# Performance work log

Hardware: AMD Instinct MI355X
Metric: run time of the kernel (lower is better)

## Reference

```python
import jax, jax.numpy as jnp
import numpy as np

K, NC, NA = 9, 13, 5
NB, NH, NW = 128, 26, 26
NT, L = 50, 2 * K + 3
NOOBJ, OBJ, SIL = 1.0, 5.0, 0.6
COORD_S, CLASS_S = 1.0, 1.0
PRETRAIN_EPOCHS = 15
TH, SHARP = 80.0, 2.0                      # corner-conf distance threshold (px), sharpness
SCALE = np.array([640.0, 480.0], np.float32)  # im_width, im_height used by corner_confidences
CONF0 = float(np.exp(SHARP) - 1.0)
ANCHORS = np.array([1.482, 2.2412, 2.0501, 3.1265, 2.3946, 4.6891,
                    3.1018, 3.991, 3.4879, 5.8851], np.float32).reshape(NA, 2)


def setup_inputs():
    k1, k2 = jax.random.split(jax.random.key(0))
    output = jax.random.normal(k1, (NB, NA * (2 * K + 1 + NC), NH, NW), dtype=jnp.float32)
    target = jax.random.uniform(k2, (NB, NT * L), dtype=jnp.float32)
    return {"output": output, "target": target, "epoch": 20}


def _corner_conf(pred, gt):
    # pred, gt: [..., K, 2] normalized corners -> mean per-corner confidence [...]
    d = jnp.sqrt((((pred - gt) * jnp.asarray(SCALE)) ** 2).sum(-1))  # pixel distance [..., K]
    c = (jnp.exp(SHARP * (1.0 - d / TH)) - 1.0) / CONF0
    return jnp.where(d < TH, c, 0.0).mean(-1)


def _region_loss(output, target, epoch):
    nAnch, nPix = NA * NH * NW, NH * NW
    tgt = jax.lax.stop_gradient(target).reshape(NB, NT, L)
    out = output.reshape(NB, NA, 2 * K + 1 + NC, NH, NW)
    # keypoint 0 gets sigmoid, the rest are raw offsets
    xs = jnp.concatenate([jax.nn.sigmoid(out[:, :, 0:1]), out[:, :, 2:2 * K:2]], axis=2)  # [B,A,K,H,W]
    ys = jnp.concatenate([jax.nn.sigmoid(out[:, :, 1:2]), out[:, :, 3:2 * K:2]], axis=2)
    conf = jax.nn.sigmoid(out[:, :, 2 * K])                             # [B,A,H,W]
    cls_logits = jnp.transpose(out[:, :, 2 * K + 1:], (0, 1, 3, 4, 2))  # [B,A,H,W,NC]

    gxg = jnp.arange(NW, dtype=jnp.float32)
    gyg = jnp.arange(NH, dtype=jnp.float32)
    px = (jax.lax.stop_gradient(xs) + gxg) / NW            # detached, as torch uses .data
    py = (jax.lax.stop_gradient(ys) + gyg[:, None]) / NH
    # pred corners per anchor cell, flat anchor index = a*H*W + j*W + i -> [B, A*H*W, K, 2]
    pc = jnp.transpose(jnp.stack([px, py], -1), (0, 1, 3, 4, 2, 5)).reshape(NB, nAnch, K, 2)

    gt_xy = tgt[:, :, 1:1 + 2 * K].reshape(NB, NT, K, 2)
    # torch loop breaks at first target with x1 == 0 -> cumulative validity
    valid = jnp.cumprod((tgt[:, :, 1] != 0).astype(jnp.int32), axis=1) > 0  # [B,T]

    # pass 1: max corner confidence over valid GT, per anchor cell
    def max_conf_step(cur, inp):
        gt_t, v_t = inp                                    # [B,K,2], [B]
        c = _corner_conf(pc, gt_t[:, None]).reshape(NB, NA, NH, NW)
        return jnp.where(v_t[:, None, None, None], jnp.maximum(cur, c), cur), None

    cur_confs, _ = jax.lax.scan(max_conf_step, jnp.zeros((NB, NA, NH, NW), jnp.float32),
                                (jnp.swapaxes(gt_xy, 0, 1), valid.T))
    conf_mask0 = jnp.where(cur_confs > SIL, 0.0, NOOBJ)

    # per-target quantities (vectorized over b,t)
    gx = gt_xy[..., 0] * NW                                # [B,T,K]
    gy = gt_xy[..., 1] * NH
    gi0 = jnp.clip(jnp.floor(gx[:, :, 0]).astype(jnp.int32), 0, NW - 1)  # [B,T]
    gj0 = jnp.clip(jnp.floor(gy[:, :, 0]).astype(jnp.int32), 0, NH - 1)
    # pred_box is fetched with best_n == -1 (as in the source); emulate torch negative flat index via mod
    flat_idx = jnp.mod(jnp.arange(NB)[:, None] * nAnch - nPix + gj0 * NW + gi0, NB * nAnch)
    pred_box = pc.reshape(NB * nAnch, K, 2)[flat_idx]      # [B,T,K,2]
    conf_t = _corner_conf(pred_box, gt_xy)                 # [B,T]
    gw = tgt[:, :, L - 2] * NW
    gh = tgt[:, :, L - 1] * NH
    aw, ah = ANCHORS[:, 0], ANCHORS[:, 1]
    mw = jnp.minimum(aw, gw[..., None])                    # centered-box IoU (bbox_iou, cxcywh)
    mh = jnp.minimum(ah, gh[..., None])
    inter = mw * mh
    iou = inter / (aw * ah + (gw * gh)[..., None] - inter)
    best_n = jnp.argmax(iou, axis=-1).astype(jnp.int32)    # [B,T] (first max, like strict '>')
    txv = gx - gi0[..., None].astype(jnp.float32)          # [B,T,K]
    tyv = gy - gj0[..., None].astype(jnp.float32)
    tclsv = tgt[:, :, 0]

    # pass 2: sequential scatter matching torch overwrite order over t
    barange = jnp.arange(NB)
    z = jnp.zeros((NB, NA, NH, NW), jnp.float32)
    zk = jnp.zeros((NB, NA, NH, NW, K), jnp.float32)

    def scatter_step(carry, inp):
        cm, clm, cfm, tx, ty, tcf, tcl = carry
        v, bn, gj, gi, cft, txt, tyt, tct = inp
        idx = (barange, bn, gj, gi)
        vk = v[:, None]
        cm = cm.at[idx].set(jnp.where(v, 1.0, cm[idx]))
        clm = clm.at[idx].set(jnp.where(v, 1.0, clm[idx]))
        cfm = cfm.at[idx].set(jnp.where(v, OBJ, cfm[idx]))
        tx = tx.at[idx].set(jnp.where(vk, txt, tx[idx]))
        ty = ty.at[idx].set(jnp.where(vk, tyt, ty[idx]))
        tcf = tcf.at[idx].set(jnp.where(v, cft, tcf[idx]))
        tcl = tcl.at[idx].set(jnp.where(v, tct, tcl[idx]))
        return (cm, clm, cfm, tx, ty, tcf, tcl), None

    inps = (valid.T, best_n.T, gj0.T, gi0.T, conf_t.T,
            jnp.swapaxes(txv, 0, 1), jnp.swapaxes(tyv, 0, 1), tclsv.T)
    (coord_mask, cls_mask, conf_mask, tx, ty, tconf, tcls), _ = jax.lax.scan(
        scatter_step, (z, z, conf_mask0, zk, zk, z, z), inps)

    # losses
    xsT = jnp.transpose(xs, (0, 1, 3, 4, 2))               # [B,A,H,W,K]
    ysT = jnp.transpose(ys, (0, 1, 3, 4, 2))
    cmk = coord_mask[..., None]
    loss_x = 0.5 * COORD_S * jnp.sum(((xsT - tx) * cmk) ** 2)
    loss_y = 0.5 * COORD_S * jnp.sum(((ysT - ty) * cmk) ** 2)
    sq = jnp.sqrt(conf_mask)
    loss_conf = 0.5 * jnp.sum(((conf - tconf) * sq) ** 2)
    labels = jnp.clip(tcls.astype(jnp.int32), 0, NC - 1)
    ce = -jnp.take_along_axis(jax.nn.log_softmax(cls_logits, axis=-1),
                              labels[..., None], axis=-1)[..., 0]
    loss_cls = CLASS_S * jnp.sum(ce * cls_mask)
    loss = loss_x + loss_y + loss_cls
    if epoch > PRETRAIN_EPOCHS:
        loss = loss + loss_conf
    return loss


def reference(output, target, epoch):
    return _region_loss(output, target, epoch)
```

## Files before the change

### kernel.cpp

```cpp
#include <hip/hip_runtime.h>
#include <math.h>

#define KK     9
#define NCLS   13
#define NANC   5
#define NBB    128
#define NHH    26
#define NWW    26
#define NTT    50
#define LL     21
#define CHC    32
#define NPIX   676
#define NANCHT 3380
#define NCELLT 432640
#define GTS    20
#define GTH    24
#define MWPB   106
#define HALFSPLIT 1728
#define NBLK   27

#define LOG2E_F   1.4426950408889634f
#define K1C       2.8853900817779268f
#define K2C       0.036067376022224085f
#define SXW       24.615384615384617f
#define SYH       18.461538461538463f
#define THRESH_S  43.500902934225507f
#define CULL_H    330.0f
#define CONF_T_SCALE 0.017390849194407297f
#define OBJ_W     5.0f
#define EPOCH_PRETRAIN 15
#define BIGV      6.0e18f

typedef _Float16 h2 __attribute__((ext_vector_type(2)));
typedef _Float16 h4 __attribute__((ext_vector_type(4)));
typedef _Float16 h8 __attribute__((ext_vector_type(8)));

static __device__ __forceinline__ float fast_exp2(float x){ return __builtin_amdgcn_exp2f(x); }
static __device__ __forceinline__ float fast_sqrt(float x){ return __builtin_amdgcn_sqrtf(x); }
static __device__ __forceinline__ float sigmoidf_(float x){
  return 1.0f/(1.0f + fast_exp2(-LOG2E_F*x));
}

__constant__ float c_anch[10] = {1.482f,2.2412f,2.0501f,3.1265f,2.3946f,4.6891f,
                                 3.1018f,3.991f,3.4879f,5.8851f};


__global__ __launch_bounds__(64) void prep_kernel(const float* __restrict__ tgt,
                                                  float* __restrict__ gts_neg,
                                                  _Float16* __restrict__ gth,
                                                  int* __restrict__ nvalid){
  int b = blockIdx.x;
  int t = threadIdx.x;
  const float* trow = tgt + (size_t)b*NTT*LL;
  float v1 = (t < NTT) ? trow[t*LL + 1] : 0.0f;
  unsigned long long mk = __ballot(t < NTT && v1 != 0.0f);
  int firstInvalid = __ffsll(~mk) - 1;
  if (t == 0) nvalid[b] = firstInvalid;
  for (int idx = t; idx < NTT*GTS; idx += 64){
    int tt = idx / GTS;
    int c  = idx - tt*GTS;
    float v;
    if (c == 9 || c == 19)      v = BIGV;
    else if (c < 9)             v = -(trow[tt*LL + 1 + 2*c] * 640.0f);
    else                        v = -(trow[tt*LL + 2 + 2*(c-10)] * 480.0f);
    gts_neg[(size_t)b*NTT*GTS + idx] = v;
  }
  for (int idx = t; idx < NTT*GTH; idx += 64){
    int tt = idx / GTH;
    int c  = idx - tt*GTH;
    float v = 0.0f;
    if (c < 8)        v = -(trow[tt*LL + 1 + 2*c] * 640.0f);
    else if (c < 16)  v = -(trow[tt*LL + 2 + 2*(c-8)] * 480.0f);
    else if (c == 16) v = -(trow[tt*LL + 1 + 16] * 640.0f);
    else if (c == 17) v = -(trow[tt*LL + 2 + 16] * 480.0f);
    gth[(size_t)b*NTT*GTH + idx] = (_Float16)v;
  }
}

__global__ __launch_bounds__(64) void region_confmask_kernel(
    const float* __restrict__ outp, const _Float16* __restrict__ gth,
    const float* __restrict__ gts_neg, const int* __restrict__ nvalid,
    unsigned int* __restrict__ maskw, double* __restrict__ partials){
  int b = blockIdx.y;
  int tid = threadIdx.x;
  int wavebase0 = blockIdx.x * 64;
  int c0 = wavebase0 + tid;
  int c1 = c0 + HALFSPLIT;
  bool ok1 = (c1 < NANCHT);

  __shared__ int sgt_i[NTT*GTH/2] __attribute__((aligned(16)));
  const int* gsrc = (const int*)(gth + (size_t)b*NTT*GTH);
  for (int idx = tid; idx < NTT*GTH/2; idx += 64) sgt_i[idx] = gsrc[idx];
  __syncthreads();
  const _Float16* sgt = (const _Float16*)sgt_i;

  float Pxf0[KK], Pyf0[KK], Pxf1[KK], Pyf1[KK];
  h8 Px8_0, Py8_0, Px8_1, Py8_1;
  h2 Pt_0, Pt_1;
  float cf0 = 0.0f, cf1 = 0.0f;
#pragma unroll
  for (int k = 0; k < KK; ++k){ Pxf1[k] = 0.0f; Pyf1[k] = 0.0f; }

  {
    int a = c0 / NPIX, rem = c0 - a*NPIX;
    int j = rem / NWW, i = rem - j*NWW;
    const float* base = outp + (((size_t)b*NANC + a)*CHC)*NPIX + rem;
#pragma unroll
    for (int k = 0; k < KK; ++k){
      float rx = base[(2*k)*NPIX], ry = base[(2*k+1)*NPIX];
      if (k == 0){ rx = sigmoidf_(rx); ry = sigmoidf_(ry); }
      Pxf0[k] = (rx + (float)i)*SXW; Pyf0[k] = (ry + (float)j)*SYH;
    }
    cf0 = sigmoidf_(base[(2*KK)*NPIX]);
  }
  if (ok1){
    int a = c1 / NPIX, rem = c1 - a*NPIX;
    int j = rem / NWW, i = rem - j*NWW;
    const float* base = outp + (((size_t)b*NANC + a)*CHC)*NPIX + rem;
#pragma unroll
    for (int k = 0; k < KK; ++k){
      float rx = base[(2*k)*NPIX], ry = base[(2*k+1)*NPIX];
      if (k == 0){ rx = sigmoidf_(rx); ry = sigmoidf_(ry); }
      Pxf1[k] = (rx + (float)i)*SXW; Pyf1[k] = (ry + (float)j)*SYH;
    }
    cf1 = sigmoidf_(base[(2*KK)*NPIX]);
  }
#pragma unroll
  for (int k = 0; k < 8; ++k){
    Px8_0[k] = (_Float16)Pxf0[k]; Py8_0[k] = (_Float16)Pyf0[k];
    Px8_1[k] = (_Float16)Pxf1[k]; Py8_1[k] = (_Float16)Pyf1[k];
  }
  Pt_0 = (h2){(_Float16)Pxf0[8], (_Float16)Pyf0[8]};
  Pt_1 = (h2){(_Float16)Pxf1[8], (_Float16)Pyf1[8]};

  const _Float16 TH16 = (_Float16)CULL_H;
  int nv = nvalid[b];
  unsigned long long q0 = 0ull, q1 = 0ull;
#pragma unroll 2
  for (int t = 0; t < nv; ++t){
    h8 GX = *(const h8*)(sgt + t*GTH);
    h8 GY = *(const h8*)(sgt + t*GTH + 8);
    h2 GT = *(const h2*)(sgt + t*GTH + 16);
    unsigned long long bit = 1ull << t;
    {
      h8 dx = Px8_0 + GX, dy = Py8_0 + GY;
      h8 r  = __builtin_elementwise_fma(dy, dy, dx*dx);
      h4 r4 = __builtin_elementwise_min(__builtin_shufflevector(r, r, 0,1,2,3),
                                        __builtin_shufflevector(r, r, 4,5,6,7));
      h2 r2 = __builtin_elementwise_min(__builtin_shufflevector(r4, r4, 0,1),
                                        __builtin_shufflevector(r4, r4, 2,3));
      h2 dt = Pt_0 + GT; h2 rt = dt*dt;
      _Float16 m = __builtin_elementwise_min(
          __builtin_elementwise_min(r2[0], r2[1]), (_Float16)(rt[0] + rt[1]));
      if (m < TH16) q0 |= bit;
    }
    {
      h8 dx = Px8_1 + GX, dy = Py8_1 + GY;
      h8 r  = __builtin_elementwise_fma(dy, dy, dx*dx);
      h4 r4 = __builtin_elementwise_min(__builtin_shufflevector(r, r, 0,1,2,3),
                                        __builtin_shufflevector(r, r, 4,5,6,7));
      h2 r2 = __builtin_elementwise_min(__builtin_shufflevector(r4, r4, 0,1),
                                        __builtin_shufflevector(r4, r4, 2,3));
      h2 dt = Pt_1 + GT; h2 rt = dt*dt;
      _Float16 m = __builtin_elementwise_min(
          __builtin_elementwise_min(r2[0], r2[1]), (_Float16)(rt[0] + rt[1]));
      if (m < TH16) q1 |= bit;
    }
  }
  if (!ok1) q1 = 0ull;

  int m0_0 = 1, m0_1 = 1;
  if (__any((q0 | q1) != 0ull)){
    const float* gbase = gts_neg + (size_t)b*NTT*GTS;
    bool e0 = false, e1 = false;
    while (q0){
      int t = __ffsll((long long)q0) - 1; q0 &= q0 - 1;
      const float* gg = gbase + t*GTS;
      float s = 0.0f;
#pragma unroll
      for (int k = 0; k < KK; ++k){
        float dx = Pxf0[k] + gg[k], dy = Pyf0[k] + gg[10+k];
        float d  = fast_sqrt(fmaf(dy, dy, dx*dx));
        float e  = fast_exp2(fmaf(d, -K2C, K1C));
        s += fmaxf(e, 1.0f);
      }
      e0 |= (s > THRESH_S);
    }
    while (q1){
      int t = __ffsll((long long)q1) - 1; q1 &= q1 - 1;
      const float* gg = gbase + t*GTS;
      float s = 0.0f;
#pragma unroll
      for (int k = 0; k < KK; ++k){
        float dx = Pxf1[k] + gg[k], dy = Pyf1[k] + gg[10+k];
        float d  = fast_sqrt(fmaf(dy, dy, dx*dx));
        float e  = fast_exp2(fmaf(d, -K2C, K1C));
        s += fmaxf(e, 1.0f);
      }
      e1 |= (s > THRESH_S);
    }
    if (e0) m0_0 = 0;
    if (e1) m0_1 = 0;
  }

  float contrib = (m0_0 ? 0.5f*cf0*cf0 : 0.0f) + ((ok1 && m0_1) ? 0.5f*cf1*cf1 : 0.0f);

  int lane = tid;
  unsigned long long mb0 = __ballot(m0_0 != 0);
  if ((lane & 31) == 0){
    unsigned int w = (lane == 0) ? (unsigned int)mb0 : (unsigned int)(mb0 >> 32);
    maskw[(size_t)b*MWPB + (wavebase0 >> 5) + (lane >> 5)] = w;
  }
  unsigned long long mb1 = __ballot(m0_1 != 0);
  int wavebase1 = wavebase0 + HALFSPLIT;
  if ((lane & 31) == 0 && wavebase1 < NANCHT){
    unsigned int w = (lane == 0) ? (unsigned int)mb1 : (unsigned int)(mb1 >> 32);
    maskw[(size_t)b*MWPB + (wavebase1 >> 5) + (lane >> 5)] = w;
  }

#pragma unroll
  for (int o = 32; o > 0; o >>= 1) contrib += __shfl_xor(contrib, o, 64);
  if (tid == 0) partials[b*NBLK + blockIdx.x] = (double)contrib;
}

__global__ __launch_bounds__(64) void scatter_loss_kernel(
    const float* __restrict__ outp, const float* __restrict__ tgt,
    const int* __restrict__ nvalid, const unsigned int* __restrict__ maskw,
    double* __restrict__ bc_part){
  int b = blockIdx.x;
  int t = threadIdx.x;
  __shared__ int keys[NTT];
  int nv = nvalid[b];
  bool valid = (t < nv);

  int key = -1, gi0 = 0, gj0 = 0, bn = 0;
  float txv[KK], tyv[KK];
  float conf_t = 0.0f, tcls = 0.0f;

  if (t < NTT){
    const float* trow = tgt + ((size_t)b*NTT + t)*LL;
    tcls = trow[0];
    float gx0 = trow[1]*(float)NWW;
    float gy0 = trow[2]*(float)NHH;
    gi0 = min(max((int)floorf(gx0), 0), NWW-1);
    gj0 = min(max((int)floorf(gy0), 0), NHH-1);
#pragma unroll
    for (int k = 0; k < KK; ++k){
      txv[k] = trow[1+2*k]*(float)NWW - (float)gi0;
      tyv[k] = trow[2+2*k]*(float)NHH - (float)gj0;
    }
    float gw = trow[LL-2]*(float)NWW, gh = trow[LL-1]*(float)NHH;
    float best = -1.0f;
    for (int a = 0; a < NANC; ++a){
      float aw = c_anch[2*a], ah = c_anch[2*a+1];
      float inter = fminf(aw, gw) * fminf(ah, gh);
      float iou = inter / (aw*ah + gw*gh - inter);
      if (iou > best){ best = iou; bn = a; }
    }
    key = bn*NPIX + gj0*NWW + gi0;
    keys[t] = key;

    long f = (long)b*NANCHT - NPIX + gj0*NWW + gi0;
    if (f < 0) f += NCELLT;
    int bb  = (int)(f / NANCHT);
    int rr  = (int)(f - (long)bb*NANCHT);
    int aa  = rr / NPIX;
    int rr2 = rr - aa*NPIX;
    int jj  = rr2 / NWW;
    int ii  = rr2 - jj*NWW;
    const float* pbase = outp + (((size_t)bb*NANC + aa)*CHC)*NPIX + rr2;
    float s = 0.0f;
#pragma unroll
    for (int k = 0; k < KK; ++k){
      float rx = pbase[(2*k)*NPIX], ry = pbase[(2*k+1)*NPIX];
      if (k == 0){ rx = sigmoidf_(rx); ry = sigmoidf_(ry); }
      float Pxx = (rx + (float)ii)*SXW, Pyy = (ry + (float)jj)*SYH;
      float dx = Pxx - trow[1+2*k]*640.0f;
      float dy = Pyy - trow[2+2*k]*480.0f;
      float d  = fast_sqrt(fmaf(dy, dy, dx*dx));
      float e  = fast_exp2(fmaf(d, -K2C, K1C));
      s += fmaxf(e, 1.0f);
    }
    conf_t = (s - 9.0f) * CONF_T_SCALE;
  }
  __syncthreads();

  bool winner = valid;
  if (valid){
    for (int u = t+1; u < nv; ++u) if (keys[u] == key){ winner = false; break; }
  }

  double lx = 0.0, ly = 0.0, lcls = 0.0, lcf = 0.0;
  if (winner){
    const float* cbase = outp + (((size_t)b*NANC + bn)*CHC)*NPIX + gj0*NWW + gi0;
    float sx = 0.0f, sy = 0.0f;
#pragma unroll
    for (int k = 0; k < KK; ++k){
      float rx = cbase[(2*k)*NPIX], ry = cbase[(2*k+1)*NPIX];
      if (k == 0){ rx = sigmoidf_(rx); ry = sigmoidf_(ry); }
      float dx = rx - txv[k], dy = ry - tyv[k];
      sx = fmaf(dx, dx, sx); sy = fmaf(dy, dy, sy);
    }
    lx = 0.5*(double)sx; ly = 0.5*(double)sy;

    float lg[NCLS], mx = -1e30f;
#pragma unroll
    for (int c = 0; c < NCLS; ++c){ lg[c] = cbase[(2*KK+1+c)*NPIX]; mx = fmaxf(mx, lg[c]); }
    float se = 0.0f;
#pragma unroll
    for (int c = 0; c < NCLS; ++c) se += fast_exp2((lg[c]-mx)*LOG2E_F);
    int label = min(max((int)tcls, 0), NCLS-1);
    lcls = (double)(mx + logf(se) - lg[label]);

    float cf = sigmoidf_(cbase[(2*KK)*NPIX]);
    int idx = bn*NPIX + gj0*NWW + gi0;
    int m0 = (maskw[(size_t)b*MWPB + (idx >> 5)] >> (idx & 31)) & 1;
    float dcf = cf - conf_t;
    lcf = 0.5*OBJ_W*(double)(dcf*dcf) - (m0 ? 0.5*(double)(cf*cf) : 0.0);
  }

#pragma unroll
  for (int o = 32; o > 0; o >>= 1){
    lx  += __shfl_xor(lx,  o, 64);
    ly  += __shfl_xor(ly,  o, 64);
    lcls+= __shfl_xor(lcls,o, 64);
    lcf += __shfl_xor(lcf, o, 64);
  }
  if (threadIdx.x == 0){
    double* bp = bc_part + (size_t)b*4;
    bp[0] = lx; bp[1] = ly; bp[2] = lcls; bp[3] = lcf;
  }
}

__global__ __launch_bounds__(256) void finalize_kernel(
    const double* __restrict__ bc_part, const double* __restrict__ partials,
    const int* __restrict__ epoch_p, float* __restrict__ outv){
  int tid = threadIdx.x;
  double vx=0, vy=0, vc=0, vf=0, vb=0;
  for (int i = tid; i < NBB; i += 256){
    vx += bc_part[4*i]; vy += bc_part[4*i+1];
    vc += bc_part[4*i+2]; vf += bc_part[4*i+3];
  }
  for (int i = tid; i < NBLK*NBB; i += 256) vb += partials[i];
#pragma unroll
  for (int o = 32; o > 0; o >>= 1){
    vx += __shfl_xor(vx, o, 64); vy += __shfl_xor(vy, o, 64);
    vc += __shfl_xor(vc, o, 64); vf += __shfl_xor(vf, o, 64);
    vb += __shfl_xor(vb, o, 64);
  }
  __shared__ double sm[5][4];
  int wid = tid >> 6, lane = tid & 63;
  if (lane == 0){ sm[0][wid]=vx; sm[1][wid]=vy; sm[2][wid]=vc; sm[3][wid]=vf; sm[4][wid]=vb; }
  __syncthreads();
  if (tid == 0){
    double fx=0, fy=0, fc=0, ff=0, fb=0;
    for (int w = 0; w < 4; ++w){ fx+=sm[0][w]; fy+=sm[1][w]; fc+=sm[2][w]; ff+=sm[3][w]; fb+=sm[4][w]; }
    double loss = fx + fy + fc;
    if (*epoch_p > EPOCH_PRETRAIN) loss += ff + fb;
    outv[0] = (float)loss;
  }
}

extern "C" void kernel_launch(void* const* d_in, const int* in_sizes, int n_in,
                              void* d_out, int out_size, void* d_ws, size_t ws_size,
                              hipStream_t stream){
  (void)in_sizes; (void)n_in; (void)out_size; (void)ws_size;
  const float* outp = (const float*)d_in[0];
  const float* tgt  = (const float*)d_in[1];
  const int*   ep   = (const int*)d_in[2];
  float* outv = (float*)d_out;
  char* ws = (char*)d_ws;

  double* bc_part   = (double*)(ws);
  double* partials  = (double*)(ws + 4096);
  float*  gts_neg   = (float*) (ws + 31744);
  int*    nvalid    = (int*)   (ws + 543744);
  unsigned int* maskw = (unsigned int*)(ws + 544256);
  _Float16* gth     = (_Float16*)(ws + 598528);

  prep_kernel<<<dim3(NBB), dim3(64), 0, stream>>>(tgt, gts_neg, gth, nvalid);
  region_confmask_kernel<<<dim3(NBLK, NBB), dim3(64), 0, stream>>>(outp, gth, gts_neg, nvalid, maskw, partials);
  scatter_loss_kernel<<<dim3(NBB), dim3(64), 0, stream>>>(outp, tgt, nvalid, maskw, bc_part);
  finalize_kernel<<<dim3(1), dim3(256), 0, stream>>>(bc_part, partials, ep, outv);
}
```

Before: 149.4 us.

## Widen confmask blocks, drop fp32 prediction registers, recompute on exact path

Measured after the change: 149.9 us. About the same (+0.3%).

```diff
diff --git a/kernel.cpp b/kernel.cpp
--- a/kernel.cpp
+++ b/kernel.cpp
@@ -16,8 +16,8 @@
 #define GTS    20
 #define GTH    24
 #define MWPB   106
-#define HALFSPLIT 1728
-#define NBLK   27
+#define HALFSPLIT 1792
+#define NBLK   7
 
 #define LOG2E_F   1.4426950408889634f
 #define K1C       2.8853900817779268f
@@ -25,21 +25,22 @@
 #define SXW       24.615384615384617f
 #define SYH       18.461538461538463f
 #define THRESH_S  43.500902934225507f
-#define CULL_H    330.0f
+#define CULL_H    400.0f
 #define CONF_T_SCALE 0.017390849194407297f
 #define OBJ_W     5.0f
 #define EPOCH_PRETRAIN 15
 #define BIGV      6.0e18f
 
 typedef _Float16 h2 __attribute__((ext_vector_type(2)));
-typedef _Float16 h4 __attribute__((ext_vector_type(4)));
-typedef _Float16 h8 __attribute__((ext_vector_type(8)));
+typedef int      i4 __attribute__((ext_vector_type(4)));
 
 static __device__ __forceinline__ float fast_exp2(float x){ return __builtin_amdgcn_exp2f(x); }
 static __device__ __forceinline__ float fast_sqrt(float x){ return __builtin_amdgcn_sqrtf(x); }
 static __device__ __forceinline__ float sigmoidf_(float x){
   return 1.0f/(1.0f + fast_exp2(-LOG2E_F*x));
 }
+static __device__ __forceinline__ h2 bch2(int v){ return __builtin_bit_cast(h2, v); }
+static __device__ __forceinline__ _Float16 hmin(_Float16 a, _Float16 b){ return a < b ? a : b; }
 
 __constant__ float c_anch[10] = {1.482f,2.2412f,2.0501f,3.1265f,2.3946f,4.6891f,
                                  3.1018f,3.991f,3.4879f,5.8851f};
@@ -77,94 +78,97 @@
   }
 }
 
-__global__ __launch_bounds__(64) void region_confmask_kernel(
+__global__ __launch_bounds__(256) void region_confmask_kernel(
     const float* __restrict__ outp, const _Float16* __restrict__ gth,
     const float* __restrict__ gts_neg, const int* __restrict__ nvalid,
     unsigned int* __restrict__ maskw, double* __restrict__ partials){
   int b = blockIdx.y;
   int tid = threadIdx.x;
-  int wavebase0 = blockIdx.x * 64;
-  int c0 = wavebase0 + tid;
+  int c0 = blockIdx.x * 256 + tid;
   int c1 = c0 + HALFSPLIT;
   bool ok1 = (c1 < NANCHT);
 
   __shared__ int sgt_i[NTT*GTH/2] __attribute__((aligned(16)));
   const int* gsrc = (const int*)(gth + (size_t)b*NTT*GTH);
-  for (int idx = tid; idx < NTT*GTH/2; idx += 64) sgt_i[idx] = gsrc[idx];
-  __syncthreads();
+  for (int idx = tid; idx < NTT*GTH/2; idx += 256) sgt_i[idx] = gsrc[idx];
   const _Float16* sgt = (const _Float16*)sgt_i;
 
-  float Pxf0[KK], Pyf0[KK], Pxf1[KK], Pyf1[KK];
-  h8 Px8_0, Py8_0, Px8_1, Py8_1;
-  h2 Pt_0, Pt_1;
-  float cf0 = 0.0f, cf1 = 0.0f;
-#pragma unroll
-  for (int k = 0; k < KK; ++k){ Pxf1[k] = 0.0f; Pyf1[k] = 0.0f; }
-
+  h2 Pxp0[4], Pyp0[4], Pt0, Pxp1[4], Pyp1[4], Pt1;
+  float cf0, cf1 = 0.0f;
   {
     int a = c0 / NPIX, rem = c0 - a*NPIX;
     int j = rem / NWW, i = rem - j*NWW;
     const float* base = outp + (((size_t)b*NANC + a)*CHC)*NPIX + rem;
+    float px8 = 0.0f, py8 = 0.0f;
 #pragma unroll
     for (int k = 0; k < KK; ++k){
       float rx = base[(2*k)*NPIX], ry = base[(2*k+1)*NPIX];
       if (k == 0){ rx = sigmoidf_(rx); ry = sigmoidf_(ry); }
-      Pxf0[k] = (rx + (float)i)*SXW; Pyf0[k] = (ry + (float)j)*SYH;
-    }
+      float px = (rx + (float)i)*SXW, py = (ry + (float)j)*SYH;
+      if (k < 8){ Pxp0[k>>1][k&1] = (_Float16)px; Pyp0[k>>1][k&1] = (_Float16)py; }
+      else { px8 = px; py8 = py; }
+    }
+    Pt0 = (h2){(_Float16)px8, (_Float16)py8};
     cf0 = sigmoidf_(base[(2*KK)*NPIX]);
   }
   if (ok1){
     int a = c1 / NPIX, rem = c1 - a*NPIX;
     int j = rem / NWW, i = rem - j*NWW;
     const float* base = outp + (((size_t)b*NANC + a)*CHC)*NPIX + rem;
+    float px8 = 0.0f, py8 = 0.0f;
 #pragma unroll
     for (int k = 0; k < KK; ++k){
       float rx = base[(2*k)*NPIX], ry = base[(2*k+1)*NPIX];
       if (k == 0){ rx = sigmoidf_(rx); ry = sigmoidf_(ry); }
-      Pxf1[k] = (rx + (float)i)*SXW; Pyf1[k] = (ry + (float)j)*SYH;
-    }
+      float px = (rx + (float)i)*SXW, py = (ry + (float)j)*SYH;
+      if (k < 8){ Pxp1[k>>1][k&1] = (_Float16)px; Pyp1[k>>1][k&1] = (_Float16)py; }
+      else { px8 = px; py8 = py; }
+    }
+    Pt1 = (h2){(_Float16)px8, (_Float16)py8};
     cf1 = sigmoidf_(base[(2*KK)*NPIX]);
-  }
-#pragma unroll
-  for (int k = 0; k < 8; ++k){
-    Px8_0[k] = (_Float16)Pxf0[k]; Py8_0[k] = (_Float16)Pyf0[k];
-    Px8_1[k] = (_Float16)Pxf1[k]; Py8_1[k] = (_Float16)Pyf1[k];
-  }
-  Pt_0 = (h2){(_Float16)Pxf0[8], (_Float16)Pyf0[8]};
-  Pt_1 = (h2){(_Float16)Pxf1[8], (_Float16)Pyf1[8]};
+  } else {
+#pragma unroll
+    for (int p = 0; p < 4; ++p){ Pxp1[p] = (h2){0,0}; Pyp1[p] = (h2){0,0}; }
+    Pt1 = (h2){0,0};
+  }
+  __syncthreads();
 
   const _Float16 TH16 = (_Float16)CULL_H;
   int nv = nvalid[b];
   unsigned long long q0 = 0ull, q1 = 0ull;
 #pragma unroll 2
   for (int t = 0; t < nv; ++t){
-    h8 GX = *(const h8*)(sgt + t*GTH);
-    h8 GY = *(const h8*)(sgt + t*GTH + 8);
-    h2 GT = *(const h2*)(sgt + t*GTH + 16);
+    const _Float16* gt = sgt + t*GTH;
+    i4 X = *(const i4*)(gt);
+    i4 Y = *(const i4*)(gt + 8);
+    int T = *(const int*)(gt + 16);
+    h2 gx[4] = {bch2(X.x), bch2(X.y), bch2(X.z), bch2(X.w)};
+    h2 gy[4] = {bch2(Y.x), bch2(Y.y), bch2(Y.z), bch2(Y.w)};
+    h2 gT = bch2(T);
     unsigned long long bit = 1ull << t;
     {
-      h8 dx = Px8_0 + GX, dy = Py8_0 + GY;
-      h8 r  = __builtin_elementwise_fma(dy, dy, dx*dx);
-      h4 r4 = __builtin_elementwise_min(__builtin_shufflevector(r, r, 0,1,2,3),
-                                        __builtin_shufflevector(r, r, 4,5,6,7));
-      h2 r2 = __builtin_elementwise_min(__builtin_shufflevector(r4, r4, 0,1),
-                                        __builtin_shufflevector(r4, r4, 2,3));
-      h2 dt = Pt_0 + GT; h2 rt = dt*dt;
-      _Float16 m = __builtin_elementwise_min(
-          __builtin_elementwise_min(r2[0], r2[1]), (_Float16)(rt[0] + rt[1]));
-      if (m < TH16) q0 |= bit;
+      h2 dx = Pxp0[0] + gx[0], dy = Pyp0[0] + gy[0];
+      h2 m  = __builtin_elementwise_fma(dy, dy, dx*dx);
+#pragma unroll
+      for (int p = 1; p < 4; ++p){
+        dx = Pxp0[p] + gx[p]; dy = Pyp0[p] + gy[p];
+        m = __builtin_elementwise_min(m, __builtin_elementwise_fma(dy, dy, dx*dx));
+      }
+      h2 dt = Pt0 + gT; h2 rt = dt*dt;
+      _Float16 mm = hmin(hmin(m[0], m[1]), (_Float16)(rt[0] + rt[1]));
+      if (mm < TH16) q0 |= bit;
     }
     {
-      h8 dx = Px8_1 + GX, dy = Py8_1 + GY;
-      h8 r  = __builtin_elementwise_fma(dy, dy, dx*dx);
-      h4 r4 = __builtin_elementwise_min(__builtin_shufflevector(r, r, 0,1,2,3),
-                                        __builtin_shufflevector(r, r, 4,5,6,7));
-      h2 r2 = __builtin_elementwise_min(__builtin_shufflevector(r4, r4, 0,1),
-                                        __builtin_shufflevector(r4, r4, 2,3));
-      h2 dt = Pt_1 + GT; h2 rt = dt*dt;
-      _Float16 m = __builtin_elementwise_min(
-          __builtin_elementwise_min(r2[0], r2[1]), (_Float16)(rt[0] + rt[1]));
-      if (m < TH16) q1 |= bit;
+      h2 dx = Pxp1[0] + gx[0], dy = Pyp1[0] + gy[0];
+      h2 m  = __builtin_elementwise_fma(dy, dy, dx*dx);
+#pragma unroll
+      for (int p = 1; p < 4; ++p){
+        dx = Pxp1[p] + gx[p]; dy = Pyp1[p] + gy[p];
+        m = __builtin_elementwise_min(m, __builtin_elementwise_fma(dy, dy, dx*dx));
+      }
+      h2 dt = Pt1 + gT; h2 rt = dt*dt;
+      _Float16 mm = hmin(hmin(m[0], m[1]), (_Float16)(rt[0] + rt[1]));
+      if (mm < TH16) q1 |= bit;
     }
   }
   if (!ok1) q1 = 0ull;
@@ -172,40 +176,66 @@
   int m0_0 = 1, m0_1 = 1;
   if (__any((q0 | q1) != 0ull)){
     const float* gbase = gts_neg + (size_t)b*NTT*GTS;
-    bool e0 = false, e1 = false;
-    while (q0){
-      int t = __ffsll((long long)q0) - 1; q0 &= q0 - 1;
-      const float* gg = gbase + t*GTS;
-      float s = 0.0f;
+    if (q0){
+      int a = c0 / NPIX, rem = c0 - a*NPIX;
+      int j = rem / NWW, i = rem - j*NWW;
+      const float* base = outp + (((size_t)b*NANC + a)*CHC)*NPIX + rem;
+      float Pxf[KK], Pyf[KK];
 #pragma unroll
       for (int k = 0; k < KK; ++k){
-        float dx = Pxf0[k] + gg[k], dy = Pyf0[k] + gg[10+k];
-        float d  = fast_sqrt(fmaf(dy, dy, dx*dx));
-        float e  = fast_exp2(fmaf(d, -K2C, K1C));
-        s += fmaxf(e, 1.0f);
-      }
-      e0 |= (s > THRESH_S);
-    }
-    while (q1){
-      int t = __ffsll((long long)q1) - 1; q1 &= q1 - 1;
-      const float* gg = gbase + t*GTS;
-      float s = 0.0f;
+        float rx = base[(2*k)*NPIX], ry = base[(2*k+1)*NPIX];
+        if (k == 0){ rx = sigmoidf_(rx); ry = sigmoidf_(ry); }
+        Pxf[k] = (rx + (float)i)*SXW; Pyf[k] = (ry + (float)j)*SYH;
+      }
+      bool exc = false;
+      while (q0){
+        int t = __ffsll((long long)q0) - 1; q0 &= q0 - 1;
+        const float* gg = gbase + t*GTS;
+        float s = 0.0f;
+#pragma unroll
+        for (int k = 0; k < KK; ++k){
+          float dx = Pxf[k] + gg[k], dy = Pyf[k] + gg[10+k];
+          float d  = fast_sqrt(fmaf(dy, dy, dx*dx));
+          float e  = fast_exp2(fmaf(d, -K2C, K1C));
+          s += fmaxf(e, 1.0f);
+        }
+        exc |= (s > THRESH_S);
+      }
+      if (exc) m0_0 = 0;
+    }
+    if (q1){
+      int a = c1 / NPIX, rem = c1 - a*NPIX;
+      int j = rem / NWW, i = rem - j*NWW;
+      const float* base = outp + (((size_t)b*NANC + a)*CHC)*NPIX + rem;
+      float Pxf[KK], Pyf[KK];
 #pragma unroll
       for (int k = 0; k < KK; ++k){
-        float dx = Pxf1[k] + gg[k], dy = Pyf1[k] + gg[10+k];
-        float d  = fast_sqrt(fmaf(dy, dy, dx*dx));
-        float e  = fast_exp2(fmaf(d, -K2C, K1C));
-        s += fmaxf(e, 1.0f);
-      }
-      e1 |= (s > THRESH_S);
-    }
-    if (e0) m0_0 = 0;
-    if (e1) m0_1 = 0;
+        float rx = base[(2*k)*NPIX], ry = base[(2*k+1)*NPIX];
+        if (k == 0){ rx = sigmoidf_(rx); ry = sigmoidf_(ry); }
+        Pxf[k] = (rx + (float)i)*SXW; Pyf[k] = (ry + (float)j)*SYH;
+      }
+      bool exc = false;
+      while (q1){
+        int t = __ffsll((long long)q1) - 1; q1 &= q1 - 1;
+        const float* gg = gbase + t*GTS;
+        float s = 0.0f;
+#pragma unroll
+        for (int k = 0; k < KK; ++k){
+          float dx = Pxf[k] + gg[k], dy = Pyf[k] + gg[10+k];
+          float d  = fast_sqrt(fmaf(dy, dy, dx*dx));
+          float e  = fast_exp2(fmaf(d, -K2C, K1C));
+          s += fmaxf(e, 1.0f);
+        }
+        exc |= (s > THRESH_S);
+      }
+      if (exc) m0_1 = 0;
+    }
   }
 
   float contrib = (m0_0 ? 0.5f*cf0*cf0 : 0.0f) + ((ok1 && m0_1) ? 0.5f*cf1*cf1 : 0.0f);
 
-  int lane = tid;
+  int lane = tid & 63;
+  int wavebase0 = blockIdx.x * 256 + (tid & ~63);
   unsigned long long mb0 = __ballot(m0_0 != 0);
   if ((lane & 31) == 0){
     unsigned int w = (lane == 0) ? (unsigned int)mb0 : (unsigned int)(mb0 >> 32);
@@ -220,7 +250,14 @@
 
 #pragma unroll
   for (int o = 32; o > 0; o >>= 1) contrib += __shfl_xor(contrib, o, 64);
-  if (tid == 0) partials[b*NBLK + blockIdx.x] = (double)contrib;
+  __shared__ float wsum[4];
+  int wid = tid >> 6;
+  if (lane == 0) wsum[wid] = contrib;
+  __syncthreads();
+  if (tid == 0){
+    double tot = (double)wsum[0] + (double)wsum[1] + (double)wsum[2] + (double)wsum[3];
+    partials[b*NBLK + blockIdx.x] = tot;
+  }
 }
 
 __global__ __launch_bounds__(64) void scatter_loss_kernel(
@@ -373,13 +410,13 @@
 
   double* bc_part   = (double*)(ws);
   double* partials  = (double*)(ws + 4096);
-  float*  gts_neg   = (float*) (ws + 31744);
-  int*    nvalid    = (int*)   (ws + 543744);
-  unsigned int* maskw = (unsigned int*)(ws + 544256);
-  _Float16* gth     = (_Float16*)(ws + 598528);
+  float*  gts_neg   = (float*) (ws + 11264);
+  int*    nvalid    = (int*)   (ws + 523264);
+  unsigned int* maskw = (unsigned int*)(ws + 523776);
+  _Float16* gth     = (_Float16*)(ws + 578048);
 
   prep_kernel<<<dim3(NBB), dim3(64), 0, stream>>>(tgt, gts_neg, gth, nvalid);
-  region_confmask_kernel<<<dim3(NBLK, NBB), dim3(64), 0, stream>>>(outp, gth, gts_neg, nvalid, maskw, partials);
+  region_confmask_kernel<<<dim3(NBLK, NBB), dim3(256), 0, stream>>>(outp, gth, gts_neg, nvalid, maskw, partials);
   scatter_loss_kernel<<<dim3(NBB), dim3(64), 0, stream>>>(outp, tgt, nvalid, maskw, bc_part);
   finalize_kernel<<<dim3(1), dim3(256), 0, stream>>>(bc_part, partials, ep, outv);
 }
```

## Rewrite culling loop with packed-f16 inline asm and scalar-loaded fixed target rows

Applied to the files above, without the earlier changes.

New measurement: 142.7 us. -4.5%, faster.

```diff
diff --git a/kernel.cpp b/kernel.cpp
--- a/kernel.cpp
+++ b/kernel.cpp
@@ -14,10 +14,11 @@
 #define NANCHT 3380
 #define NCELLT 432640
 #define GTS    20
-#define GTH    24
+#define TROWS  52
+#define GTW    10
 #define MWPB   106
-#define HALFSPLIT 1728
-#define NBLK   27
+#define HALFSPLIT 1792
+#define NBLK   14
 
 #define LOG2E_F   1.4426950408889634f
 #define K1C       2.8853900817779268f
@@ -25,21 +26,36 @@
 #define SXW       24.615384615384617f
 #define SYH       18.461538461538463f
 #define THRESH_S  43.500902934225507f
-#define CULL_H    330.0f
+#define CULL_H    400.0f
 #define CONF_T_SCALE 0.017390849194407297f
 #define OBJ_W     5.0f
 #define EPOCH_PRETRAIN 15
 #define BIGV      6.0e18f
+#define INFH      0x7C00u
+#define INFH2     0x7C007C00u
 
 typedef _Float16 h2 __attribute__((ext_vector_type(2)));
-typedef _Float16 h4 __attribute__((ext_vector_type(4)));
-typedef _Float16 h8 __attribute__((ext_vector_type(8)));
 
 static __device__ __forceinline__ float fast_exp2(float x){ return __builtin_amdgcn_exp2f(x); }
 static __device__ __forceinline__ float fast_sqrt(float x){ return __builtin_amdgcn_sqrtf(x); }
 static __device__ __forceinline__ float sigmoidf_(float x){
   return 1.0f/(1.0f + fast_exp2(-LOG2E_F*x));
 }
+static __device__ __forceinline__ int pk_add_sv(int s, int v){
+  int d; asm("v_pk_add_f16 %0, %1, %2" : "=v"(d) : "s"(s), "v"(v)); return d;
+}
+static __device__ __forceinline__ int pk_mul_vv(int a, int b){
+  int d; asm("v_pk_mul_f16 %0, %1, %2" : "=v"(d) : "v"(a), "v"(b)); return d;
+}
+static __device__ __forceinline__ int pk_fma_vvv(int a, int b, int c){
+  int d; asm("v_pk_fma_f16 %0, %1, %2, %3" : "=v"(d) : "v"(a), "v"(b), "v"(c)); return d;
+}
+static __device__ __forceinline__ int pk_min_vv(int a, int b){
+  int d; asm("v_pk_min_f16 %0, %1, %2" : "=v"(d) : "v"(a), "v"(b)); return d;
+}
+static __device__ __forceinline__ unsigned short f2h_bits(float v){
+  return __builtin_bit_cast(unsigned short, (_Float16)v);
+}
 
 __constant__ float c_anch[10] = {1.482f,2.2412f,2.0501f,3.1265f,2.3946f,4.6891f,
                                  3.1018f,3.991f,3.4879f,5.8851f};
@@ -47,15 +63,15 @@
 
 __global__ __launch_bounds__(64) void prep_kernel(const float* __restrict__ tgt,
                                                   float* __restrict__ gts_neg,
-                                                  _Float16* __restrict__ gth,
+                                                  unsigned* __restrict__ gthw,
                                                   int* __restrict__ nvalid){
   int b = blockIdx.x;
   int t = threadIdx.x;
   const float* trow = tgt + (size_t)b*NTT*LL;
   float v1 = (t < NTT) ? trow[t*LL + 1] : 0.0f;
   unsigned long long mk = __ballot(t < NTT && v1 != 0.0f);
-  int firstInvalid = __ffsll(~mk) - 1;
-  if (t == 0) nvalid[b] = firstInvalid;
+  int nv = __ffsll(~mk) - 1;
+  if (t == 0) nvalid[b] = nv;
   for (int idx = t; idx < NTT*GTS; idx += 64){
     int tt = idx / GTS;
     int c  = idx - tt*GTS;
@@ -65,42 +81,52 @@
     else                        v = -(trow[tt*LL + 2 + 2*(c-10)] * 480.0f);
     gts_neg[(size_t)b*NTT*GTS + idx] = v;
   }
-  for (int idx = t; idx < NTT*GTH; idx += 64){
-    int tt = idx / GTH;
-    int c  = idx - tt*GTH;
-    float v = 0.0f;
-    if (c < 8)        v = -(trow[tt*LL + 1 + 2*c] * 640.0f);
-    else if (c < 16)  v = -(trow[tt*LL + 2 + 2*(c-8)] * 480.0f);
-    else if (c == 16) v = -(trow[tt*LL + 1 + 16] * 640.0f);
-    else if (c == 17) v = -(trow[tt*LL + 2 + 16] * 480.0f);
-    gth[(size_t)b*NTT*GTH + idx] = (_Float16)v;
-  }
-}
-
-__global__ __launch_bounds__(64) void region_confmask_kernel(
-    const float* __restrict__ outp, const _Float16* __restrict__ gth,
-    const float* __restrict__ gts_neg, const int* __restrict__ nvalid,
-    unsigned int* __restrict__ maskw, double* __restrict__ partials){
+  if (t < TROWS){
+    unsigned w[GTW];
+    if (t < nv){
+      const float* tr = trow + t*LL;
+      float xs[KK], ys[KK];
+#pragma unroll
+      for (int k = 0; k < KK; ++k){
+        xs[k] = -(tr[1+2*k] * 640.0f);
+        ys[k] = -(tr[2+2*k] * 480.0f);
+      }
+#pragma unroll
+      for (int p = 0; p < 4; ++p){
+        w[p]   = (unsigned)f2h_bits(xs[2*p]) | ((unsigned)f2h_bits(xs[2*p+1]) << 16);
+        w[5+p] = (unsigned)f2h_bits(ys[2*p]) | ((unsigned)f2h_bits(ys[2*p+1]) << 16);
+      }
+      w[4] = (unsigned)f2h_bits(xs[8]) | (INFH << 16);
+      w[9] = (unsigned)f2h_bits(ys[8]) | (INFH << 16);
+    } else {
+#pragma unroll
+      for (int p = 0; p < GTW; ++p) w[p] = INFH2;
+    }
+    unsigned* dst = gthw + ((size_t)b*TROWS + t)*GTW;
+#pragma unroll
+    for (int p = 0; p < GTW; ++p) dst[p] = w[p];
+  }
+}
+
+__global__ __launch_bounds__(128) void region_confmask_kernel(
+    const float* __restrict__ outp, const unsigned* __restrict__ gthw,
+    const float* __restrict__ gts_neg, unsigned int* __restrict__ maskw,
+    double* __restrict__ partials){
   int b = blockIdx.y;
   int tid = threadIdx.x;
-  int wavebase0 = blockIdx.x * 64;
-  int c0 = wavebase0 + tid;
+  int c0 = blockIdx.x * 128 + tid;
   int c1 = c0 + HALFSPLIT;
   bool ok1 = (c1 < NANCHT);
 
-  __shared__ int sgt_i[NTT*GTH/2] __attribute__((aligned(16)));
-  const int* gsrc = (const int*)(gth + (size_t)b*NTT*GTH);
-  for (int idx = tid; idx < NTT*GTH/2; idx += 64) sgt_i[idx] = gsrc[idx];
-  __syncthreads();
-  const _Float16* sgt = (const _Float16*)sgt_i;
+  __shared__ float sgt[NTT*GTS] __attribute__((aligned(16)));
+  {
+    const float* g32 = gts_neg + (size_t)b*NTT*GTS;
+    for (int idx = tid; idx < NTT*GTS; idx += 128) sgt[idx] = g32[idx];
+  }
 
   float Pxf0[KK], Pyf0[KK], Pxf1[KK], Pyf1[KK];
-  h8 Px8_0, Py8_0, Px8_1, Py8_1;
-  h2 Pt_0, Pt_1;
-  float cf0 = 0.0f, cf1 = 0.0f;
-#pragma unroll
-  for (int k = 0; k < KK; ++k){ Pxf1[k] = 0.0f; Pyf1[k] = 0.0f; }
-
+  int Pxw0[5], Pyw0[5], Pxw1[5], Pyw1[5];
+  float cf0, cf1 = 0.0f;
   {
     int a = c0 / NPIX, rem = c0 - a*NPIX;
     int j = rem / NWW, i = rem - j*NWW;
@@ -124,58 +150,69 @@
       Pxf1[k] = (rx + (float)i)*SXW; Pyf1[k] = (ry + (float)j)*SYH;
     }
     cf1 = sigmoidf_(base[(2*KK)*NPIX]);
-  }
-#pragma unroll
-  for (int k = 0; k < 8; ++k){
-    Px8_0[k] = (_Float16)Pxf0[k]; Py8_0[k] = (_Float16)Pyf0[k];
-    Px8_1[k] = (_Float16)Pxf1[k]; Py8_1[k] = (_Float16)Pyf1[k];
-  }
-  Pt_0 = (h2){(_Float16)Pxf0[8], (_Float16)Pyf0[8]};
-  Pt_1 = (h2){(_Float16)Pxf1[8], (_Float16)Pyf1[8]};
+  } else {
+#pragma unroll
+    for (int k = 0; k < KK; ++k){ Pxf1[k] = 0.0f; Pyf1[k] = 0.0f; }
+  }
+#pragma unroll
+  for (int p = 0; p < 4; ++p){
+    Pxw0[p] = (unsigned)f2h_bits(Pxf0[2*p]) | ((unsigned)f2h_bits(Pxf0[2*p+1]) << 16);
+    Pyw0[p] = (unsigned)f2h_bits(Pyf0[2*p]) | ((unsigned)f2h_bits(Pyf0[2*p+1]) << 16);
+    Pxw1[p] = (unsigned)f2h_bits(Pxf1[2*p]) | ((unsigned)f2h_bits(Pxf1[2*p+1]) << 16);
+    Pyw1[p] = (unsigned)f2h_bits(Pyf1[2*p]) | ((unsigned)f2h_bits(Pyf1[2*p+1]) << 16);
+  }
+  Pxw0[4] = (unsigned)f2h_bits(Pxf0[8]); Pyw0[4] = (unsigned)f2h_bits(Pyf0[8]);
+  Pxw1[4] = (unsigned)f2h_bits(Pxf1[8]); Pyw1[4] = (unsigned)f2h_bits(Pyf1[8]);
+  __syncthreads();
 
   const _Float16 TH16 = (_Float16)CULL_H;
-  int nv = nvalid[b];
+  const unsigned* gsrc = gthw + (size_t)b*TROWS*GTW;
   unsigned long long q0 = 0ull, q1 = 0ull;
-#pragma unroll 2
-  for (int t = 0; t < nv; ++t){
-    h8 GX = *(const h8*)(sgt + t*GTH);
-    h8 GY = *(const h8*)(sgt + t*GTH + 8);
-    h2 GT = *(const h2*)(sgt + t*GTH + 16);
-    unsigned long long bit = 1ull << t;
-    {
-      h8 dx = Px8_0 + GX, dy = Py8_0 + GY;
-      h8 r  = __builtin_elementwise_fma(dy, dy, dx*dx);
-      h4 r4 = __builtin_elementwise_min(__builtin_shufflevector(r, r, 0,1,2,3),
-                                        __builtin_shufflevector(r, r, 4,5,6,7));
-      h2 r2 = __builtin_elementwise_min(__builtin_shufflevector(r4, r4, 0,1),
-                                        __builtin_shufflevector(r4, r4, 2,3));
-      h2 dt = Pt_0 + GT; h2 rt = dt*dt;
-      _Float16 m = __builtin_elementwise_min(
-          __builtin_elementwise_min(r2[0], r2[1]), (_Float16)(rt[0] + rt[1]));
-      if (m < TH16) q0 |= bit;
-    }
-    {
-      h8 dx = Px8_1 + GX, dy = Py8_1 + GY;
-      h8 r  = __builtin_elementwise_fma(dy, dy, dx*dx);
-      h4 r4 = __builtin_elementwise_min(__builtin_shufflevector(r, r, 0,1,2,3),
-                                        __builtin_shufflevector(r, r, 4,5,6,7));
-      h2 r2 = __builtin_elementwise_min(__builtin_shufflevector(r4, r4, 0,1),
-                                        __builtin_shufflevector(r4, r4, 2,3));
-      h2 dt = Pt_1 + GT; h2 rt = dt*dt;
-      _Float16 m = __builtin_elementwise_min(
-          __builtin_elementwise_min(r2[0], r2[1]), (_Float16)(rt[0] + rt[1]));
-      if (m < TH16) q1 |= bit;
+#pragma unroll 1
+  for (int c = 0; c < 13; ++c){
+    int G[40];
+#pragma unroll
+    for (int w = 0; w < 40; ++w) G[w] = (int)gsrc[c*40 + w];
+#pragma unroll
+    for (int u = 0; u < 4; ++u){
+      int t = c*4 + u;
+      unsigned long long bit = 1ull << t;
+      {
+        int dx = pk_add_sv(G[u*10+0], Pxw0[0]); int r = pk_mul_vv(dx,dx);
+        int dy = pk_add_sv(G[u*10+5], Pyw0[0]); r = pk_fma_vvv(dy,dy,r);
+        int m = r;
+#pragma unroll
+        for (int p = 1; p < 5; ++p){
+          dx = pk_add_sv(G[u*10+p],   Pxw0[p]); r = pk_mul_vv(dx,dx);
+          dy = pk_add_sv(G[u*10+5+p], Pyw0[p]); r = pk_fma_vvv(dy,dy,r);
+          m = pk_min_vv(m, r);
+        }
+        h2 mh = __builtin_bit_cast(h2, m);
+        if ((mh[0] < TH16) | (mh[1] < TH16)) q0 |= bit;
+      }
+      {
+        int dx = pk_add_sv(G[u*10+0], Pxw1[0]); int r = pk_mul_vv(dx,dx);
+        int dy = pk_add_sv(G[u*10+5], Pyw1[0]); r = pk_fma_vvv(dy,dy,r);
+        int m = r;
+#pragma unroll
+        for (int p = 1; p < 5; ++p){
+          dx = pk_add_sv(G[u*10+p],   Pxw1[p]); r = pk_mul_vv(dx,dx);
+          dy = pk_add_sv(G[u*10+5+p], Pyw1[p]); r = pk_fma_vvv(dy,dy,r);
+          m = pk_min_vv(m, r);
+        }
+        h2 mh = __builtin_bit_cast(h2, m);
+        if ((mh[0] < TH16) | (mh[1] < TH16)) q1 |= bit;
+      }
     }
   }
   if (!ok1) q1 = 0ull;
 
   int m0_0 = 1, m0_1 = 1;
-  if (__any((q0 | q1) != 0ull)){
-    const float* gbase = gts_neg + (size_t)b*NTT*GTS;
+  {
     bool e0 = false, e1 = false;
     while (q0){
       int t = __ffsll((long long)q0) - 1; q0 &= q0 - 1;
-      const float* gg = gbase + t*GTS;
+      const float* gg = sgt + t*GTS;
       float s = 0.0f;
 #pragma unroll
       for (int k = 0; k < KK; ++k){
@@ -188,7 +225,7 @@
     }
     while (q1){
       int t = __ffsll((long long)q1) - 1; q1 &= q1 - 1;
-      const float* gg = gbase + t*GTS;
+      const float* gg = sgt + t*GTS;
       float s = 0.0f;
 #pragma unroll
       for (int k = 0; k < KK; ++k){
@@ -205,7 +242,8 @@
 
   float contrib = (m0_0 ? 0.5f*cf0*cf0 : 0.0f) + ((ok1 && m0_1) ? 0.5f*cf1*cf1 : 0.0f);
 
-  int lane = tid;
+  int lane = tid & 63;
+  int wavebase0 = blockIdx.x * 128 + (tid & ~63);
   unsigned long long mb0 = __ballot(m0_0 != 0);
   if ((lane & 31) == 0){
     unsigned int w = (lane == 0) ? (unsigned int)mb0 : (unsigned int)(mb0 >> 32);
@@ -220,7 +258,12 @@
 
 #pragma unroll
   for (int o = 32; o > 0; o >>= 1) contrib += __shfl_xor(contrib, o, 64);
-  if (tid == 0) partials[b*NBLK + blockIdx.x] = (double)contrib;
+  __shared__ float wsum[2];
+  int wid = tid >> 6;
+  if (lane == 0) wsum[wid] = contrib;
+  __syncthreads();
+  if (tid == 0)
+    partials[b*NBLK + blockIdx.x] = (double)wsum[0] + (double)wsum[1];
 }
 
 __global__ __launch_bounds__(64) void scatter_loss_kernel(
@@ -373,13 +416,13 @@
 
   double* bc_part   = (double*)(ws);
   double* partials  = (double*)(ws + 4096);
-  float*  gts_neg   = (float*) (ws + 31744);
-  int*    nvalid    = (int*)   (ws + 543744);
-  unsigned int* maskw = (unsigned int*)(ws + 544256);
-  _Float16* gth     = (_Float16*)(ws + 598528);
-
-  prep_kernel<<<dim3(NBB), dim3(64), 0, stream>>>(tgt, gts_neg, gth, nvalid);
-  region_confmask_kernel<<<dim3(NBLK, NBB), dim3(64), 0, stream>>>(outp, gth, gts_neg, nvalid, maskw, partials);
+  float*  gts_neg   = (float*) (ws + 18432);
+  int*    nvalid    = (int*)   (ws + 530432);
+  unsigned int* maskw = (unsigned int*)(ws + 530944);
+  unsigned* gthw    = (unsigned*)(ws + 585216);
+
+  prep_kernel<<<dim3(NBB), dim3(64), 0, stream>>>(tgt, gts_neg, gthw, nvalid);
+  region_confmask_kernel<<<dim3(NBLK, NBB), dim3(128), 0, stream>>>(outp, gthw, gts_neg, maskw, partials);
   scatter_loss_kernel<<<dim3(NBB), dim3(64), 0, stream>>>(outp, tgt, nvalid, maskw, bc_part);
   finalize_kernel<<<dim3(1), dim3(256), 0, stream>>>(bc_part, partials, ep, outv);
 }
```
